# Kernel optimization log

Measured on AMD Instinct MI355X. Metric: run time of the kernel, lower is better.

The kernel has to match this reference:

```python
import jax, jax.numpy as jnp
import numpy as np
from jax import lax

NPOINT = 1024
RADIUS = 0.2
NSAMPLE = 32
BN_EPS = 1e-5


def _gather(points, idx):
    # points [B,N,C], idx [B,S] or [B,S,K] -> [B,S,C] / [B,S,K,C]
    return jax.vmap(lambda p, i: p[i])(points, idx)


def farthest_point_sample(xyz, npoint):
    # xyz [B,N,3] -> idx [B,npoint]; deterministic start at index 0
    B, N, _ = xyz.shape

    def step(carry, _):
        distance, farthest = carry
        centroid = jnp.take_along_axis(xyz, farthest[:, None, None], axis=1)  # [B,1,3]
        dist = jnp.sum((xyz - centroid) ** 2, axis=-1)  # [B,N]
        distance = jnp.minimum(distance, dist)
        nxt = jnp.argmax(distance, axis=1).astype(jnp.int32)
        return (distance, nxt), farthest

    init = (jnp.full((B, N), 1e10, xyz.dtype), jnp.zeros((B,), jnp.int32))
    _, cents = lax.scan(step, init, None, length=npoint)  # [npoint,B]
    return cents.T  # [B,npoint]


def query_ball_point(radius, nsample, xyz, new_xyz):
    # xyz [B,N,3], new_xyz [B,S,3] -> idx [B,S,nsample]
    B, N, _ = xyz.shape
    sqrdists = (jnp.sum(new_xyz ** 2, -1, keepdims=True)
                - 2.0 * jnp.einsum('bsc,bnc->bsn', new_xyz, xyz)
                + jnp.sum(xyz ** 2, -1)[:, None, :])  # [B,S,N]
    idx = jnp.where(sqrdists > radius * radius, N, jnp.arange(N, dtype=jnp.int32)[None, None, :])
    idx = jnp.sort(idx, axis=-1)[:, :, :nsample]
    first = idx[:, :, :1]
    idx = jnp.where(idx == N, first, idx)
    return jnp.minimum(idx, N - 1)


def _mlp_bn_relu_stack(x, params):
    # x [B,S,K,C]; 1x1 conv == per-point linear; BN in training mode (batch stats)
    for (w, b, g, bt) in params:
        x = jnp.einsum('bskc,oc->bsko', x, w) + b
        mean = jnp.mean(x, axis=(0, 1, 2))
        var = jnp.var(x, axis=(0, 1, 2))
        x = g * (x - mean) * lax.rsqrt(var + BN_EPS) + bt
        x = jax.nn.relu(x)
    return x


def setup_inputs() -> dict:
    key = jax.random.key(0)
    ks = jax.random.split(key, 8)
    B, N, D = 16, 4096, 64
    xyz = jax.random.uniform(ks[0], (B, N, 3), dtype=jnp.float32)
    points = jax.random.normal(ks[1], (B, N, D), dtype=jnp.float32)
    chans = [67, 64, 64, 128]
    inp = {"xyz": xyz, "points": points}
    for i in range(3):
        cin, cout = chans[i], chans[i + 1]
        inp[f"w{i+1}"] = jax.random.normal(ks[2 + i], (cout, cin), dtype=jnp.float32) * 0.05
        inp[f"b{i+1}"] = jnp.zeros((cout,), jnp.float32)
        inp[f"g{i+1}"] = jnp.ones((cout,), jnp.float32)
        inp[f"bt{i+1}"] = jnp.zeros((cout,), jnp.float32)
    return inp


def reference(xyz, points, w1, b1, g1, bt1, w2, b2, g2, bt2, w3, b3, g3, bt3):
    B, N, _ = xyz.shape
    fps_idx = farthest_point_sample(xyz, NPOINT)  # [B,S]
    new_xyz = _gather(xyz, fps_idx)  # [B,S,3]
    gidx = query_ball_point(RADIUS, NSAMPLE, xyz, new_xyz)  # [B,S,K]
    grouped_xyz = _gather(xyz, gidx) - new_xyz[:, :, None, :]  # [B,S,K,3]
    feat = jnp.concatenate([grouped_xyz, _gather(points, gidx)], axis=-1)  # [B,S,K,67]
    params = [(w1, b1, g1, bt1), (w2, b2, g2, bt2), (w3, b3, g3, bt3)]
    feat = _mlp_bn_relu_stack(feat, params)  # [B,S,K,128]
    new_points = jnp.max(feat, axis=2)  # [B,S,128]
    return (new_xyz, new_points)
```

## Files before the change

kernel.cpp:

```cpp
#include <hip/hip_runtime.h>
#include <cstdint>

#define NB 16
#define NN 4096
#define ND 64
#define NPOINT 1024
#define NSAMPLE 32
#define NROWS (NB * NPOINT * NSAMPLE)
#define BN_EPS 1e-5f
#define NSLOT 32
#define LD 68

#define OFF_GIDX   0
#define OFF_STATS  (2 * 1024 * 1024)
#define OFF_MAX    (OFF_STATS + 131072)
#define OFF_MIN    (OFF_MAX + 8388608)
#define MED_TOTAL  ((size_t)OFF_MIN + 8388608)
#define SMALL_TOTAL ((size_t)OFF_MAX)
#define OFF_Y2BF   MED_TOTAL
#define BIG_TOTAL  (OFF_Y2BF + (size_t)NROWS * 64 * 2)
#define OFF_Y1BF   BIG_TOTAL
#define BIG2_TOTAL (OFF_Y1BF + (size_t)NROWS * 64 * 2)

#define S1SUM 0
#define S1SQ  2048
#define S2SUM 4096
#define S2SQ  6144
#define S3SUM 8192
#define S3SQ  12288
#define A3OFF 16384
#define C3OFF 16512

__device__ __forceinline__ unsigned short f2bf(float f) {
    const unsigned u = __float_as_uint(f);
    return (unsigned short)((u + 0x7FFFu + ((u >> 16) & 1u)) >> 16);
}
__device__ __forceinline__ float bf2f(unsigned short s) {
    return __uint_as_float(((unsigned)s) << 16);
}

__global__ __launch_bounds__(256) void fps_kernel(const float* __restrict__ xyz,
                                                  float* __restrict__ out_newxyz) {
    __shared__ float pxyz[NN * 3];
    __shared__ unsigned long long skey[2][4];
    __shared__ float sxyz[2][4][3];
    const int b = blockIdx.x, tid = threadIdx.x;
    const int wave = tid >> 6, lane = tid & 63;
    const float* base = xyz + (size_t)b * NN * 3;

    for (int i = tid; i < NN * 3 / 4; i += 256)
        reinterpret_cast<float4*>(pxyz)[i] = reinterpret_cast<const float4*>(base)[i];
    __syncthreads();

    float X[16], Y[16], Z[16], D[16];
#pragma unroll
    for (int k = 0; k < 16; ++k) {
        const int p = k * 256 + tid;
        X[k] = pxyz[3 * p + 0];
        Y[k] = pxyz[3 * p + 1];
        Z[k] = pxyz[3 * p + 2];
        D[k] = 1e10f;
    }

    float cx = pxyz[0], cy = pxyz[1], cz = pxyz[2];
    float* outb = out_newxyz + (size_t)b * NPOINT * 3;

    for (int it = 0; it < NPOINT; ++it) {
        if (tid == 0) {
            outb[it * 3 + 0] = cx;
            outb[it * 3 + 1] = cy;
            outb[it * 3 + 2] = cz;
        }
        float bv = -1.0f;
        int   bi = 0;
#pragma unroll
        for (int k = 0; k < 16; ++k) {
            const float dx = __fsub_rn(X[k], cx);
            const float dy = __fsub_rn(Y[k], cy);
            const float dz = __fsub_rn(Z[k], cz);
            const float d  = __fadd_rn(__fadd_rn(__fmul_rn(dx, dx), __fmul_rn(dy, dy)),
                                       __fmul_rn(dz, dz));
            const float nd = fminf(D[k], d);
            D[k] = nd;
            if (nd > bv) { bv = nd; bi = k * 256 + tid; }
        }
        unsigned long long key =
            ((unsigned long long)__float_as_uint(bv) << 32) | (unsigned)(~bi);
#pragma unroll
        for (int off = 32; off >= 1; off >>= 1) {
            const unsigned long long ok = __shfl_xor(key, off);
            key = (ok > key) ? ok : key;
        }
        const int par = it & 1;
        if (lane == 0) {
            const int widx = (int)(~(unsigned)key);
            skey[par][wave] = key;
            sxyz[par][wave][0] = pxyz[3 * widx + 0];
            sxyz[par][wave][1] = pxyz[3 * widx + 1];
            sxyz[par][wave][2] = pxyz[3 * widx + 2];
        }
        __syncthreads();
        unsigned long long k0 = skey[par][0], k1 = skey[par][1];
        unsigned long long k2 = skey[par][2], k3 = skey[par][3];
        float ax = sxyz[par][0][0], ay = sxyz[par][0][1], az = sxyz[par][0][2];
        const float bx = sxyz[par][1][0], by = sxyz[par][1][1], bz = sxyz[par][1][2];
        float ex = sxyz[par][2][0], ey = sxyz[par][2][1], ez = sxyz[par][2][2];
        const float fx = sxyz[par][3][0], fy = sxyz[par][3][1], fz = sxyz[par][3][2];
        if (k1 > k0) { k0 = k1; ax = bx; ay = by; az = bz; }
        if (k3 > k2) { k2 = k3; ex = fx; ey = fy; ez = fz; }
        if (k2 > k0) { ax = ex; ay = ey; az = ez; }
        cx = ax; cy = ay; cz = az;
    }
}

__global__ __launch_bounds__(256) void query_kernel(const float* __restrict__ xyz,
                                                    const float* __restrict__ newxyz,
                                                    int* __restrict__ gidx) {
    const int gtid = blockIdx.x * 256 + threadIdx.x;
    const int q    = gtid >> 6;
    const int lane = threadIdx.x & 63;
    if (q >= NB * NPOINT) return;
    const int b = q >> 10;
    const float* xb = xyz + (size_t)b * NN * 3;
    const float cx = newxyz[q * 3 + 0];
    const float cy = newxyz[q * 3 + 1];
    const float cz = newxyz[q * 3 + 2];
    const float snew = __fadd_rn(__fadd_rn(__fmul_rn(cx, cx), __fmul_rn(cy, cy)),
                                 __fmul_rn(cz, cz));
    const float rsq = (float)(0.2 * 0.2);
    int* outq = gidx + (size_t)q * NSAMPLE;

    int count = 0, first = 0;
    for (int base = 0; base < NN; base += 128) {
        const int pA = base + lane, pB = base + 64 + lane;
        const float xA = xb[pA * 3 + 0], yA = xb[pA * 3 + 1], zA = xb[pA * 3 + 2];
        const float xB = xb[pB * 3 + 0], yB = xb[pB * 3 + 1], zB = xb[pB * 3 + 2];
        const float sxA = __fadd_rn(__fadd_rn(__fmul_rn(xA, xA), __fmul_rn(yA, yA)),
                                    __fmul_rn(zA, zA));
        const float sxB = __fadd_rn(__fadd_rn(__fmul_rn(xB, xB), __fmul_rn(yB, yB)),
                                    __fmul_rn(zB, zB));
        float dotA = __fmul_rn(cx, xA);
        dotA = fmaf(cy, yA, dotA);
        dotA = fmaf(cz, zA, dotA);
        float dotB = __fmul_rn(cx, xB);
        dotB = fmaf(cy, yB, dotB);
        dotB = fmaf(cz, zB, dotB);
        const float sqA = __fadd_rn(__fsub_rn(snew, __fadd_rn(dotA, dotA)), sxA);
        const float sqB = __fadd_rn(__fsub_rn(snew, __fadd_rn(dotB, dotB)), sxB);
        const bool qualA = !(sqA > rsq);
        const bool qualB = !(sqB > rsq);
        const unsigned long long maskA = __ballot(qualA);
        const unsigned long long maskB = __ballot(qualB);
        if (count == 0) {
            if (maskA)      first = base + (int)__builtin_ctzll(maskA);
            else if (maskB) first = base + 64 + (int)__builtin_ctzll(maskB);
        }
        const unsigned long long below = (1ull << lane) - 1ull;
        const int cA = __popcll(maskA);
        if (qualA) {
            const int pos = count + __popcll(maskA & below);
            if (pos < NSAMPLE) outq[pos] = pA;
        }
        if (qualB) {
            const int pos = count + cA + __popcll(maskB & below);
            if (pos < NSAMPLE) outq[pos] = pB;
        }
        count += cA + __popcll(maskB);
        if (count >= NSAMPLE) break;
    }
    if (count < NSAMPLE) {
        for (int pos = count + lane; pos < NSAMPLE; pos += 64) outq[pos] = first;
    }
}

__device__ __forceinline__ void stage64(const float* __restrict__ xyz,
                                        const float* __restrict__ points,
                                        const float* __restrict__ newxyz,
                                        const int* __restrict__ gidx,
                                        int row0, int tid, float* featT) {
    const int rl = tid >> 2, qd = tid & 3;
    const int R   = row0 + rl;
    const int grp = R >> 5;
    const int idx = gidx[R];
    const int b   = grp >> 10;
    const float* prow = points + ((size_t)b * NN + idx) * ND + qd * 16;
#pragma unroll
    for (int j = 0; j < 4; ++j) {
        const float4 v = *reinterpret_cast<const float4*>(prow + j * 4);
        const int k = 3 + qd * 16 + j * 4;
        featT[(k + 0) * LD + rl] = v.x;
        featT[(k + 1) * LD + rl] = v.y;
        featT[(k + 2) * LD + rl] = v.z;
        featT[(k + 3) * LD + rl] = v.w;
    }
    if (qd == 0) {
        const float* xr = xyz + ((size_t)b * NN + idx) * 3;
        const float* cr = newxyz + (size_t)grp * 3;
        featT[0 * LD + rl] = xr[0] - cr[0];
        featT[1 * LD + rl] = xr[1] - cr[1];
        featT[2 * LD + rl] = xr[2] - cr[2];
    }
}

__device__ __forceinline__ void fold64(const float* __restrict__ ssum,
                                       const float* __restrict__ ssq,
                                       const float* __restrict__ g,
                                       const float* __restrict__ bt,
                                       int tid, float* a_s, float* c_s) {
    if (tid < 64) {
        float s = 0.f, q = 0.f;
#pragma unroll
        for (int sl = 0; sl < NSLOT; ++sl) { s += ssum[sl * 64 + tid]; q += ssq[sl * 64 + tid]; }
        const float Ninv = 1.0f / (float)NROWS;
        const float mean = s * Ninv;
        const float var  = fmaf(-mean, mean, q * Ninv);
        const float a    = g[tid] * rsqrtf(var + BN_EPS);
        a_s[tid] = a;
        c_s[tid] = bt[tid] - mean * a;
    }
}

template<int CIN>
__device__ __forceinline__ void mm_bnrelu(const float* __restrict__ w,
                                          const float* __restrict__ bias,
                                          const float* inT, float* outT,
                                          const float* a_s, const float* c_s, int tid) {
    const int c = tid & 63, rg = tid >> 6;
    float wr[CIN];
#pragma unroll
    for (int k = 0; k < CIN; ++k) wr[k] = w[c * CIN + k];
    const float bv = bias[c];
    const float av = a_s[c], cv = c_s[c];
#pragma unroll
    for (int bat = 0; bat < 2; ++bat) {
        const int rb = rg * 16 + bat * 8;
        float acc[8];
#pragma unroll
        for (int j = 0; j < 8; ++j) acc[j] = bv;
#pragma unroll
        for (int k = 0; k < CIN; ++k) {
            float f[8];
            *reinterpret_cast<float4*>(&f[0]) = *reinterpret_cast<const float4*>(&inT[k * LD + rb]);
            *reinterpret_cast<float4*>(&f[4]) = *reinterpret_cast<const float4*>(&inT[k * LD + rb + 4]);
            const float wv = wr[k];
#pragma unroll
            for (int j = 0; j < 8; ++j) acc[j] = fmaf(f[j], wv, acc[j]);
        }
        float o[8];
#pragma unroll
        for (int j = 0; j < 8; ++j) o[j] = fmaxf(0.f, fmaf(av, acc[j], cv));
        *reinterpret_cast<float4*>(&outT[c * LD + rb])     = *reinterpret_cast<float4*>(&o[0]);
        *reinterpret_cast<float4*>(&outT[c * LD + rb + 4]) = *reinterpret_cast<float4*>(&o[4]);
    }
}

template<bool ST>
__global__ __launch_bounds__(256) void pass1_kernel(
    const float* __restrict__ xyz, const float* __restrict__ points,
    const float* __restrict__ newxyz, const int* __restrict__ gidx,
    const float* __restrict__ w1, const float* __restrict__ b1,
    float* __restrict__ stats, unsigned short* __restrict__ y1bf) {
    __shared__ float featT[67 * LD];
    __shared__ float red[4][64], redq[4][64];
    const int tid = threadIdx.x, blk = blockIdx.x;
    stage64(xyz, points, newxyz, gidx, blk * 64, tid, featT);
    __syncthreads();
    const int c = tid & 63, rg = tid >> 6;
    float wr[67];
#pragma unroll
    for (int k = 0; k < 67; ++k) wr[k] = w1[c * 67 + k];
    const float bv = b1[c];
    float ssum = 0.f, ssq = 0.f;
#pragma unroll
    for (int bat = 0; bat < 2; ++bat) {
        const int rb = rg * 16 + bat * 8;
        float acc[8];
#pragma unroll
        for (int j = 0; j < 8; ++j) acc[j] = bv;
#pragma unroll
        for (int k = 0; k < 67; ++k) {
            float f[8];
            *reinterpret_cast<float4*>(&f[0]) = *reinterpret_cast<const float4*>(&featT[k * LD + rb]);
            *reinterpret_cast<float4*>(&f[4]) = *reinterpret_cast<const float4*>(&featT[k * LD + rb + 4]);
            const float wv = wr[k];
#pragma unroll
            for (int j = 0; j < 8; ++j) acc[j] = fmaf(f[j], wv, acc[j]);
        }
        if (ST) {
            unsigned short o[8];
#pragma unroll
            for (int j = 0; j < 8; ++j) o[j] = f2bf(acc[j]);
            *reinterpret_cast<uint4*>(&y1bf[(size_t)blk * 4096 + c * 64 + rb]) =
                *reinterpret_cast<uint4*>(o);
        }
#pragma unroll
        for (int j = 0; j < 8; ++j) { ssum += acc[j]; ssq = fmaf(acc[j], acc[j], ssq); }
    }
    red[rg][c] = ssum;
    redq[rg][c] = ssq;
    __syncthreads();
    if (tid < 64) {
        const float s = red[0][tid] + red[1][tid] + red[2][tid] + red[3][tid];
        const float q = redq[0][tid] + redq[1][tid] + redq[2][tid] + redq[3][tid];
        const int slot = blk & (NSLOT - 1);
        atomicAdd(&stats[S1SUM + slot * 64 + tid], s);
        atomicAdd(&stats[S1SQ + slot * 64 + tid], q);
    }
}

__global__ __launch_bounds__(256) void pass2big_kernel(
    const unsigned short* __restrict__ y1bf,
    const float* __restrict__ g1, const float* __restrict__ bt1,
    const float* __restrict__ w2, const float* __restrict__ b2,
    float* __restrict__ stats, unsigned short* __restrict__ y2bf) {
    __shared__ float t1T[64 * LD];
    __shared__ float a1s[64], c1s[64];
    __shared__ float red[4][64], redq[4][64];
    const int tid = threadIdx.x, blk = blockIdx.x;
    fold64(stats + S1SUM, stats + S1SQ, g1, bt1, tid, a1s, c1s);
    __syncthreads();
    {
        const int cch = tid >> 2, r0 = (tid & 3) * 16;
        const float a1 = a1s[cch], c1 = c1s[cch];
        const uint4 u0 = *reinterpret_cast<const uint4*>(&y1bf[(size_t)blk * 4096 + cch * 64 + r0]);
        const uint4 u1 = *reinterpret_cast<const uint4*>(&y1bf[(size_t)blk * 4096 + cch * 64 + r0 + 8]);
        const unsigned short* us0 = reinterpret_cast<const unsigned short*>(&u0);
        const unsigned short* us1 = reinterpret_cast<const unsigned short*>(&u1);
#pragma unroll
        for (int j = 0; j < 8; ++j) {
            t1T[cch * LD + r0 + j]     = fmaxf(0.f, fmaf(a1, bf2f(us0[j]), c1));
            t1T[cch * LD + r0 + 8 + j] = fmaxf(0.f, fmaf(a1, bf2f(us1[j]), c1));
        }
    }
    __syncthreads();
    const int c = tid & 63, rg = tid >> 6;
    float wr[64];
#pragma unroll
    for (int k = 0; k < 64; ++k) wr[k] = w2[c * 64 + k];
    const float bv = b2[c];
    float ssum = 0.f, ssq = 0.f;
#pragma unroll
    for (int bat = 0; bat < 2; ++bat) {
        const int rb = rg * 16 + bat * 8;
        float acc[8];
#pragma unroll
        for (int j = 0; j < 8; ++j) acc[j] = bv;
#pragma unroll
        for (int k = 0; k < 64; ++k) {
            float f[8];
            *reinterpret_cast<float4*>(&f[0]) = *reinterpret_cast<const float4*>(&t1T[k * LD + rb]);
            *reinterpret_cast<float4*>(&f[4]) = *reinterpret_cast<const float4*>(&t1T[k * LD + rb + 4]);
            const float wv = wr[k];
#pragma unroll
            for (int j = 0; j < 8; ++j) acc[j] = fmaf(f[j], wv, acc[j]);
        }
        {
            unsigned short o[8];
#pragma unroll
            for (int j = 0; j < 8; ++j) o[j] = f2bf(acc[j]);
            *reinterpret_cast<uint4*>(&y2bf[(size_t)blk * 4096 + c * 64 + rb]) =
                *reinterpret_cast<uint4*>(o);
        }
#pragma unroll
        for (int j = 0; j < 8; ++j) { ssum += acc[j]; ssq = fmaf(acc[j], acc[j], ssq); }
    }
    red[rg][c] = ssum;
    redq[rg][c] = ssq;
    __syncthreads();
    if (tid < 64) {
        const float s = red[0][tid] + red[1][tid] + red[2][tid] + red[3][tid];
        const float q = redq[0][tid] + redq[1][tid] + redq[2][tid] + redq[3][tid];
        const int slot = blk & (NSLOT - 1);
        atomicAdd(&stats[S2SUM + slot * 64 + tid], s);
        atomicAdd(&stats[S2SQ + slot * 64 + tid], q);
    }
}

template<bool ST>
__global__ __launch_bounds__(256) void pass2_kernel(
    const float* __restrict__ xyz, const float* __restrict__ points,
    const float* __restrict__ newxyz, const int* __restrict__ gidx,
    const float* __restrict__ w1, const float* __restrict__ b1,
    const float* __restrict__ g1, const float* __restrict__ bt1,
    const float* __restrict__ w2, const float* __restrict__ b2,
    float* __restrict__ stats, unsigned short* __restrict__ y2bf) {
    __shared__ float featT[67 * LD];
    __shared__ float t1T[64 * LD];
    __shared__ float a1s[64], c1s[64];
    __shared__ float red[4][64], redq[4][64];
    const int tid = threadIdx.x, blk = blockIdx.x;
    fold64(stats + S1SUM, stats + S1SQ, g1, bt1, tid, a1s, c1s);
    stage64(xyz, points, newxyz, gidx, blk * 64, tid, featT);
    __syncthreads();
    mm_bnrelu<67>(w1, b1, featT, t1T, a1s, c1s, tid);
    __syncthreads();
    const int c = tid & 63, rg = tid >> 6;
    float wr[64];
#pragma unroll
    for (int k = 0; k < 64; ++k) wr[k] = w2[c * 64 + k];
    const float bv = b2[c];
    float ssum = 0.f, ssq = 0.f;
#pragma unroll
    for (int bat = 0; bat < 2; ++bat) {
        const int rb = rg * 16 + bat * 8;
        float acc[8];
#pragma unroll
        for (int j = 0; j < 8; ++j) acc[j] = bv;
#pragma unroll
        for (int k = 0; k < 64; ++k) {
            float f[8];
            *reinterpret_cast<float4*>(&f[0]) = *reinterpret_cast<const float4*>(&t1T[k * LD + rb]);
            *reinterpret_cast<float4*>(&f[4]) = *reinterpret_cast<const float4*>(&t1T[k * LD + rb + 4]);
            const float wv = wr[k];
#pragma unroll
            for (int j = 0; j < 8; ++j) acc[j] = fmaf(f[j], wv, acc[j]);
        }
        if (ST) {
            unsigned short o[8];
#pragma unroll
            for (int j = 0; j < 8; ++j) o[j] = f2bf(acc[j]);
            *reinterpret_cast<uint4*>(&y2bf[(size_t)blk * 4096 + c * 64 + rb]) =
                *reinterpret_cast<uint4*>(o);
        }
#pragma unroll
        for (int j = 0; j < 8; ++j) { ssum += acc[j]; ssq = fmaf(acc[j], acc[j], ssq); }
    }
    red[rg][c] = ssum;
    redq[rg][c] = ssq;
    __syncthreads();
    if (tid < 64) {
        const float s = red[0][tid] + red[1][tid] + red[2][tid] + red[3][tid];
        const float q = redq[0][tid] + redq[1][tid] + redq[2][tid] + redq[3][tid];
        const int slot = blk & (NSLOT - 1);
        atomicAdd(&stats[S2SUM + slot * 64 + tid], s);
        atomicAdd(&stats[S2SQ + slot * 64 + tid], q);
    }
}

__global__ __launch_bounds__(256) void pass3big_kernel(
    const unsigned short* __restrict__ y2bf,
    const float* __restrict__ g2, const float* __restrict__ bt2,
    const float* __restrict__ w3, const float* __restrict__ b3,
    float* __restrict__ stats, float* __restrict__ maxbuf, float* __restrict__ minbuf) {
    __shared__ float t2T[64 * LD];
    __shared__ float a2s[64], c2s[64];
    __shared__ float redM[4][128], redm[4][128], redS[4][128], redQ[4][128];
    const int tid = threadIdx.x, blk = blockIdx.x;
    fold64(stats + S2SUM, stats + S2SQ, g2, bt2, tid, a2s, c2s);
    __syncthreads();
    {
        const int cch = tid >> 2, r0 = (tid & 3) * 16;
        const float a2 = a2s[cch], c2 = c2s[cch];
        const uint4 u0 = *reinterpret_cast<const uint4*>(&y2bf[(size_t)blk * 4096 + cch * 64 + r0]);
        const uint4 u1 = *reinterpret_cast<const uint4*>(&y2bf[(size_t)blk * 4096 + cch * 64 + r0 + 8]);
        const unsigned short* us0 = reinterpret_cast<const unsigned short*>(&u0);
        const unsigned short* us1 = reinterpret_cast<const unsigned short*>(&u1);
#pragma unroll
        for (int j = 0; j < 8; ++j) {
            t2T[cch * LD + r0 + j]     = fmaxf(0.f, fmaf(a2, bf2f(us0[j]), c2));
            t2T[cch * LD + r0 + 8 + j] = fmaxf(0.f, fmaf(a2, bf2f(us1[j]), c2));
        }
    }
    __syncthreads();

    const int c0 = tid & 63, rg2 = tid >> 6;
    const int rb = rg2 * 16;
    float acc0[16], acc1[16];
    const float bv0 = b3[c0], bv1 = b3[c0 + 64];
#pragma unroll
    for (int j = 0; j < 16; ++j) { acc0[j] = bv0; acc1[j] = bv1; }
    for (int half = 0; half < 2; ++half) {
        float wr0[32], wr1[32];
#pragma unroll
        for (int k = 0; k < 32; ++k) {
            wr0[k] = w3[c0 * 64 + half * 32 + k];
            wr1[k] = w3[(c0 + 64) * 64 + half * 32 + k];
        }
#pragma unroll
        for (int k = 0; k < 32; ++k) {
            const int kk = half * 32 + k;
            float f[16];
            *reinterpret_cast<float4*>(&f[0])  = *reinterpret_cast<const float4*>(&t2T[kk * LD + rb]);
            *reinterpret_cast<float4*>(&f[4])  = *reinterpret_cast<const float4*>(&t2T[kk * LD + rb + 4]);
            *reinterpret_cast<float4*>(&f[8])  = *reinterpret_cast<const float4*>(&t2T[kk * LD + rb + 8]);
            *reinterpret_cast<float4*>(&f[12]) = *reinterpret_cast<const float4*>(&t2T[kk * LD + rb + 12]);
            const float w0 = wr0[k], w1v = wr1[k];
#pragma unroll
            for (int j = 0; j < 16; ++j) {
                acc0[j] = fmaf(f[j], w0, acc0[j]);
                acc1[j] = fmaf(f[j], w1v, acc1[j]);
            }
        }
    }
    float maxv0 = -3.4e38f, minv0 = 3.4e38f, ssum0 = 0.f, ssq0 = 0.f;
    float maxv1 = -3.4e38f, minv1 = 3.4e38f, ssum1 = 0.f, ssq1 = 0.f;
#pragma unroll
    for (int j = 0; j < 16; ++j) {
        maxv0 = fmaxf(maxv0, acc0[j]); minv0 = fminf(minv0, acc0[j]);
        ssum0 += acc0[j]; ssq0 = fmaf(acc0[j], acc0[j], ssq0);
        maxv1 = fmaxf(maxv1, acc1[j]); minv1 = fminf(minv1, acc1[j]);
        ssum1 += acc1[j]; ssq1 = fmaf(acc1[j], acc1[j], ssq1);
    }
    redM[rg2][c0] = maxv0; redM[rg2][c0 + 64] = maxv1;
    redm[rg2][c0] = minv0; redm[rg2][c0 + 64] = minv1;
    redS[rg2][c0] = ssum0; redS[rg2][c0 + 64] = ssum1;
    redQ[rg2][c0] = ssq0;  redQ[rg2][c0 + 64] = ssq1;
    __syncthreads();
    {
        const int g2i = tid >> 7, cc = tid & 127;
        const int g = blk * 2 + g2i;
        maxbuf[(size_t)g * 128 + cc] = fmaxf(redM[2 * g2i][cc], redM[2 * g2i + 1][cc]);
        minbuf[(size_t)g * 128 + cc] = fminf(redm[2 * g2i][cc], redm[2 * g2i + 1][cc]);
    }
    if (tid < 128) {
        const float s = (redS[0][tid] + redS[1][tid]) + (redS[2][tid] + redS[3][tid]);
        const float q = (redQ[0][tid] + redQ[1][tid]) + (redQ[2][tid] + redQ[3][tid]);
        const int slot = blk & (NSLOT - 1);
        atomicAdd(&stats[S3SUM + slot * 128 + tid], s);
        atomicAdd(&stats[S3SQ + slot * 128 + tid], q);
    }
}

template<bool MM>
__global__ __launch_bounds__(256) void pass3_kernel(
    const float* __restrict__ xyz, const float* __restrict__ points,
    const float* __restrict__ newxyz, const int* __restrict__ gidx,
    const float* __restrict__ w1, const float* __restrict__ b1,
    const float* __restrict__ g1, const float* __restrict__ bt1,
    const float* __restrict__ w2, const float* __restrict__ b2,
    const float* __restrict__ g2, const float* __restrict__ bt2,
    const float* __restrict__ w3, const float* __restrict__ b3,
    float* __restrict__ stats, float* __restrict__ maxbuf, float* __restrict__ minbuf) {
    __shared__ float bufA[67 * LD];
    __shared__ float t1T[64 * LD];
    __shared__ float a1s[64], c1s[64], a2s[64], c2s[64];
    __shared__ float redM[4][128], redm[4][128], redS[4][128], redQ[4][128];
    const int tid = threadIdx.x, blk = blockIdx.x;
    fold64(stats + S1SUM, stats + S1SQ, g1, bt1, tid, a1s, c1s);
    fold64(stats + S2SUM, stats + S2SQ, g2, bt2, tid, a2s, c2s);
    stage64(xyz, points, newxyz, gidx, blk * 64, tid, bufA);
    __syncthreads();
    mm_bnrelu<67>(w1, b1, bufA, t1T, a1s, c1s, tid);
    __syncthreads();
    mm_bnrelu<64>(w2, b2, t1T, bufA, a2s, c2s, tid);
    __syncthreads();

    const int c0 = tid & 63, rg2 = tid >> 6;
    const int rb = rg2 * 16;
    float acc0[16], acc1[16];
    const float bv0 = b3[c0], bv1 = b3[c0 + 64];
#pragma unroll
    for (int j = 0; j < 16; ++j) { acc0[j] = bv0; acc1[j] = bv1; }
    for (int half = 0; half < 2; ++half) {
        float wr0[32], wr1[32];
#pragma unroll
        for (int k = 0; k < 32; ++k) {
            wr0[k] = w3[c0 * 64 + half * 32 + k];
            wr1[k] = w3[(c0 + 64) * 64 + half * 32 + k];
        }
#pragma unroll
        for (int k = 0; k < 32; ++k) {
            const int kk = half * 32 + k;
            float f[16];
            *reinterpret_cast<float4*>(&f[0])  = *reinterpret_cast<const float4*>(&bufA[kk * LD + rb]);
            *reinterpret_cast<float4*>(&f[4])  = *reinterpret_cast<const float4*>(&bufA[kk * LD + rb + 4]);
            *reinterpret_cast<float4*>(&f[8])  = *reinterpret_cast<const float4*>(&bufA[kk * LD + rb + 8]);
            *reinterpret_cast<float4*>(&f[12]) = *reinterpret_cast<const float4*>(&bufA[kk * LD + rb + 12]);
            const float w0 = wr0[k], w1v = wr1[k];
#pragma unroll
            for (int j = 0; j < 16; ++j) {
                acc0[j] = fmaf(f[j], w0, acc0[j]);
                acc1[j] = fmaf(f[j], w1v, acc1[j]);
            }
        }
    }
    float maxv0 = -3.4e38f, minv0 = 3.4e38f, ssum0 = 0.f, ssq0 = 0.f;
    float maxv1 = -3.4e38f, minv1 = 3.4e38f, ssum1 = 0.f, ssq1 = 0.f;
#pragma unroll
    for (int j = 0; j < 16; ++j) {
        maxv0 = fmaxf(maxv0, acc0[j]); minv0 = fminf(minv0, acc0[j]);
        ssum0 += acc0[j]; ssq0 = fmaf(acc0[j], acc0[j], ssq0);
        maxv1 = fmaxf(maxv1, acc1[j]); minv1 = fminf(minv1, acc1[j]);
        ssum1 += acc1[j]; ssq1 = fmaf(acc1[j], acc1[j], ssq1);
    }
    redM[rg2][c0] = maxv0; redM[rg2][c0 + 64] = maxv1;
    redm[rg2][c0] = minv0; redm[rg2][c0 + 64] = minv1;
    redS[rg2][c0] = ssum0; redS[rg2][c0 + 64] = ssum1;
    redQ[rg2][c0] = ssq0;  redQ[rg2][c0 + 64] = ssq1;
    __syncthreads();
    if (MM) {
        const int g2i = tid >> 7, cc = tid & 127;
        const int g = blk * 2 + g2i;
        maxbuf[(size_t)g * 128 + cc] = fmaxf(redM[2 * g2i][cc], redM[2 * g2i + 1][cc]);
        minbuf[(size_t)g * 128 + cc] = fminf(redm[2 * g2i][cc], redm[2 * g2i + 1][cc]);
    }
    if (tid < 128) {
        const float s = (redS[0][tid] + redS[1][tid]) + (redS[2][tid] + redS[3][tid]);
        const float q = (redQ[0][tid] + redQ[1][tid]) + (redQ[2][tid] + redQ[3][tid]);
        const int slot = blk & (NSLOT - 1);
        atomicAdd(&stats[S3SUM + slot * 128 + tid], s);
        atomicAdd(&stats[S3SQ + slot * 128 + tid], q);
    }
}

__global__ __launch_bounds__(256) void pass4_kernel(
    const float* __restrict__ xyz, const float* __restrict__ points,
    const float* __restrict__ newxyz, const int* __restrict__ gidx,
    const float* __restrict__ w1, const float* __restrict__ b1,
    const float* __restrict__ g1, const float* __restrict__ bt1,
    const float* __restrict__ w2, const float* __restrict__ b2,
    const float* __restrict__ g2, const float* __restrict__ bt2,
    const float* __restrict__ w3, const float* __restrict__ b3,
    const float* __restrict__ g3, const float* __restrict__ bt3,
    const float* __restrict__ stats, float* __restrict__ outp) {
    __shared__ float bufA[67 * LD];
    __shared__ float t1T[64 * LD];
    __shared__ float a1s[64], c1s[64], a2s[64], c2s[64];
    __shared__ float a3s[128], c3s[128];
    const int tid = threadIdx.x, blk = blockIdx.x;
    fold64(stats + S1SUM, stats + S1SQ, g1, bt1, tid, a1s, c1s);
    fold64(stats + S2SUM, stats + S2SQ, g2, bt2, tid, a2s, c2s);
    if (tid < 128) {
        float s = 0.f, q = 0.f;
#pragma unroll
        for (int sl = 0; sl < NSLOT; ++sl) { s += stats[S3SUM + sl * 128 + tid]; q += stats[S3SQ + sl * 128 + tid]; }
        const float Ninv = 1.0f / (float)NROWS;
        const float mean = s * Ninv;
        const float var  = fmaf(-mean, mean, q * Ninv);
        const float a    = g3[tid] * rsqrtf(var + BN_EPS);
        a3s[tid] = a;
        c3s[tid] = bt3[tid] - mean * a;
    }
    stage64(xyz, points, newxyz, gidx, blk * 64, tid, bufA);
    __syncthreads();
    mm_bnrelu<67>(w1, b1, bufA, t1T, a1s, c1s, tid);
    __syncthreads();
    mm_bnrelu<64>(w2, b2, t1T, bufA, a2s, c2s, tid);
    __syncthreads();

    const int c2 = tid & 127, rg2 = tid >> 7;
    float wr[64];
#pragma unroll
    for (int k = 0; k < 64; ++k) wr[k] = w3[c2 * 64 + k];
    const float bv = b3[c2];
    const float av = a3s[c2], cv = c3s[c2];
    float maxv = -3.4e38f;
#pragma unroll
    for (int bat = 0; bat < 4; ++bat) {
        const int rb = rg2 * 32 + bat * 8;
        float acc[8];
#pragma unroll
        for (int j = 0; j < 8; ++j) acc[j] = bv;
#pragma unroll
        for (int k = 0; k < 64; ++k) {
            float f[8];
            *reinterpret_cast<float4*>(&f[0]) = *reinterpret_cast<const float4*>(&bufA[k * LD + rb]);
            *reinterpret_cast<float4*>(&f[4]) = *reinterpret_cast<const float4*>(&bufA[k * LD + rb + 4]);
            const float wv = wr[k];
#pragma unroll
            for (int j = 0; j < 8; ++j) acc[j] = fmaf(f[j], wv, acc[j]);
        }
#pragma unroll
        for (int j = 0; j < 8; ++j) maxv = fmaxf(maxv, fmaxf(0.f, fmaf(av, acc[j], cv)));
    }
    const int g = blk * 2 + rg2;
    outp[(size_t)g * 128 + c2] = maxv;
}

__global__ void derive3_kernel(const float* __restrict__ g3, const float* __restrict__ bt3,
                               float* __restrict__ stats) {
    const int c = threadIdx.x;
    float s = 0.f, q = 0.f;
#pragma unroll
    for (int sl = 0; sl < NSLOT; ++sl) { s += stats[S3SUM + sl * 128 + c]; q += stats[S3SQ + sl * 128 + c]; }
    const float Ninv = 1.0f / (float)NROWS;
    const float mean = s * Ninv;
    const float var  = fmaf(-mean, mean, q * Ninv);
    const float a    = g3[c] * rsqrtf(var + BN_EPS);
    stats[A3OFF + c] = a;
    stats[C3OFF + c] = bt3[c] - mean * a;
}

__global__ __launch_bounds__(256) void final_kernel(
    const float* __restrict__ maxbuf, const float* __restrict__ minbuf,
    const float* __restrict__ stats, float* __restrict__ outp) {
    const int gid = blockIdx.x * 256 + threadIdx.x;
    if (gid >= NB * NPOINT * 128) return;
    const int c = gid & 127;
    const float a  = stats[A3OFF + c];
    const float cc = stats[C3OFF + c];
    const float v  = (a >= 0.f) ? maxbuf[gid] : minbuf[gid];
    outp[gid] = fmaxf(0.f, fmaf(a, v, cc));
}

extern "C" void kernel_launch(void* const* d_in, const int* in_sizes, int n_in,
                              void* d_out, int out_size, void* d_ws, size_t ws_size,
                              hipStream_t stream) {
    const float* xyz    = (const float*)d_in[0];
    const float* points = (const float*)d_in[1];
    const float* w1 = (const float*)d_in[2];
    const float* b1 = (const float*)d_in[3];
    const float* g1 = (const float*)d_in[4];
    const float* bt1 = (const float*)d_in[5];
    const float* w2 = (const float*)d_in[6];
    const float* b2 = (const float*)d_in[7];
    const float* g2 = (const float*)d_in[8];
    const float* bt2 = (const float*)d_in[9];
    const float* w3 = (const float*)d_in[10];
    const float* b3 = (const float*)d_in[11];
    const float* g3 = (const float*)d_in[12];
    const float* bt3 = (const float*)d_in[13];

    float* out_newxyz = (float*)d_out;
    float* out_newpts = (float*)d_out + NB * NPOINT * 3;

    char* ws = (char*)d_ws;
    if (ws_size < SMALL_TOTAL) return;

    int*   gidx   = (int*)(ws + OFF_GIDX);
    float* stats  = (float*)(ws + OFF_STATS);
    float* maxbuf = (float*)(ws + OFF_MAX);
    float* minbuf = (float*)(ws + OFF_MIN);
    unsigned short* y2bf = (unsigned short*)(ws + OFF_Y2BF);
    unsigned short* y1bf = (unsigned short*)(ws + OFF_Y1BF);
    const bool med  = (ws_size >= MED_TOTAL);
    const bool big  = (ws_size >= BIG_TOTAL);
    const bool big2 = (ws_size >= BIG2_TOTAL);

    hipMemsetAsync(stats, 0, 65536, stream);

    fps_kernel<<<NB, 256, 0, stream>>>(xyz, out_newxyz);
    query_kernel<<<(NB * NPOINT * 64) / 256, 256, 0, stream>>>(xyz, out_newxyz, gidx);
    if (big2) {
        pass1_kernel<true><<<NROWS / 64, 256, 0, stream>>>(xyz, points, out_newxyz, gidx,
                                                           w1, b1, stats, y1bf);
        pass2big_kernel<<<NROWS / 64, 256, 0, stream>>>(y1bf, g1, bt1, w2, b2, stats, y2bf);
        pass3big_kernel<<<NROWS / 64, 256, 0, stream>>>(y2bf, g2, bt2, w3, b3,
                                                        stats, maxbuf, minbuf);
        derive3_kernel<<<1, 128, 0, stream>>>(g3, bt3, stats);
        final_kernel<<<(NB * NPOINT * 128) / 256, 256, 0, stream>>>(maxbuf, minbuf, stats, out_newpts);
    } else if (big) {
        pass1_kernel<false><<<NROWS / 64, 256, 0, stream>>>(xyz, points, out_newxyz, gidx,
                                                            w1, b1, stats, y1bf);
        pass2_kernel<true><<<NROWS / 64, 256, 0, stream>>>(xyz, points, out_newxyz, gidx,
                                                           w1, b1, g1, bt1, w2, b2, stats, y2bf);
        pass3big_kernel<<<NROWS / 64, 256, 0, stream>>>(y2bf, g2, bt2, w3, b3,
                                                        stats, maxbuf, minbuf);
        derive3_kernel<<<1, 128, 0, stream>>>(g3, bt3, stats);
        final_kernel<<<(NB * NPOINT * 128) / 256, 256, 0, stream>>>(maxbuf, minbuf, stats, out_newpts);
    } else if (med) {
        pass1_kernel<false><<<NROWS / 64, 256, 0, stream>>>(xyz, points, out_newxyz, gidx,
                                                            w1, b1, stats, y1bf);
        pass2_kernel<false><<<NROWS / 64, 256, 0, stream>>>(xyz, points, out_newxyz, gidx,
                                                            w1, b1, g1, bt1, w2, b2, stats, y2bf);
        pass3_kernel<true><<<NROWS / 64, 256, 0, stream>>>(xyz, points, out_newxyz, gidx,
                                                           w1, b1, g1, bt1, w2, b2, g2, bt2,
                                                           w3, b3, stats, maxbuf, minbuf);
        derive3_kernel<<<1, 128, 0, stream>>>(g3, bt3, stats);
        final_kernel<<<(NB * NPOINT * 128) / 256, 256, 0, stream>>>(maxbuf, minbuf, stats, out_newpts);
    } else {
        pass1_kernel<false><<<NROWS / 64, 256, 0, stream>>>(xyz, points, out_newxyz, gidx,
                                                            w1, b1, stats, y1bf);
        pass2_kernel<false><<<NROWS / 64, 256, 0, stream>>>(xyz, points, out_newxyz, gidx,
                                                            w1, b1, g1, bt1, w2, b2, stats, y2bf);
        pass3_kernel<false><<<NROWS / 64, 256, 0, stream>>>(xyz, points, out_newxyz, gidx,
                                                            w1, b1, g1, bt1, w2, b2, g2, bt2,
                                                            w3, b3, stats, maxbuf, minbuf);
        pass4_kernel<<<NROWS / 64, 256, 0, stream>>>(xyz, points, out_newxyz, gidx,
                                                     w1, b1, g1, bt1, w2, b2, g2, bt2,
                                                     w3, b3, g3, bt3, stats, out_newpts);
    }
}
```

Baseline: 1.193 ms.

## Widen FPS block to 512 threads and simplify per-iteration argmax reduction

The farthest-point-sampling kernel now runs 512 threads per batch, so each thread holds 8 points, assigned contiguously, instead of 16 strided ones. The 64-bit key shuffle reduction becomes a float max shuffle followed by a ballot and lane lookup. Each wave publishes one float4 slot, and every thread scans 8 slots to pick the winner. This shortens the serial per-iteration chain in the 1024-step loop. It may change tie-breaking: lowest lane first, and a strict greater-than across waves favours lower waves. Contiguous indexing keeps lowest-index ties in order.

```diff
diff --git a/kernel.cpp b/kernel.cpp
--- a/kernel.cpp
+++ b/kernel.cpp
@@ -39,23 +39,22 @@
     return __uint_as_float(((unsigned)s) << 16);
 }
 
-__global__ __launch_bounds__(256) void fps_kernel(const float* __restrict__ xyz,
+__global__ __launch_bounds__(512) void fps_kernel(const float* __restrict__ xyz,
                                                   float* __restrict__ out_newxyz) {
     __shared__ float pxyz[NN * 3];
-    __shared__ unsigned long long skey[2][4];
-    __shared__ float sxyz[2][4][3];
+    __shared__ float4 slot[2][8];
     const int b = blockIdx.x, tid = threadIdx.x;
     const int wave = tid >> 6, lane = tid & 63;
     const float* base = xyz + (size_t)b * NN * 3;
 
-    for (int i = tid; i < NN * 3 / 4; i += 256)
+    for (int i = tid; i < NN * 3 / 4; i += 512)
         reinterpret_cast<float4*>(pxyz)[i] = reinterpret_cast<const float4*>(base)[i];
     __syncthreads();
 
-    float X[16], Y[16], Z[16], D[16];
-#pragma unroll
-    for (int k = 0; k < 16; ++k) {
-        const int p = k * 256 + tid;
+    float X[8], Y[8], Z[8], D[8];
+#pragma unroll
+    for (int k = 0; k < 8; ++k) {
+        const int p = tid * 8 + k;
         X[k] = pxyz[3 * p + 0];
         Y[k] = pxyz[3 * p + 1];
         Z[k] = pxyz[3 * p + 2];
@@ -74,7 +73,7 @@
         float bv = -1.0f;
         int   bi = 0;
 #pragma unroll
-        for (int k = 0; k < 16; ++k) {
+        for (int k = 0; k < 8; ++k) {
             const float dx = __fsub_rn(X[k], cx);
             const float dy = __fsub_rn(Y[k], cy);
             const float dz = __fsub_rn(Z[k], cz);
@@ -82,34 +81,29 @@
                                        __fmul_rn(dz, dz));
             const float nd = fminf(D[k], d);
             D[k] = nd;
-            if (nd > bv) { bv = nd; bi = k * 256 + tid; }
-        }
-        unsigned long long key =
-            ((unsigned long long)__float_as_uint(bv) << 32) | (unsigned)(~bi);
-#pragma unroll
-        for (int off = 32; off >= 1; off >>= 1) {
-            const unsigned long long ok = __shfl_xor(key, off);
-            key = (ok > key) ? ok : key;
-        }
+            if (nd > bv) { bv = nd; bi = tid * 8 + k; }
+        }
+        const float lv = bv;
+#pragma unroll
+        for (int off = 32; off >= 1; off >>= 1)
+            bv = fmaxf(bv, __shfl_xor(bv, off));
+        const unsigned long long mask = __ballot(lv == bv);
+        const int src  = (int)__builtin_ctzll(mask);
+        const int widx = __shfl(bi, src);
         const int par = it & 1;
         if (lane == 0) {
-            const int widx = (int)(~(unsigned)key);
-            skey[par][wave] = key;
-            sxyz[par][wave][0] = pxyz[3 * widx + 0];
-            sxyz[par][wave][1] = pxyz[3 * widx + 1];
-            sxyz[par][wave][2] = pxyz[3 * widx + 2];
+            slot[par][wave] = make_float4(bv, pxyz[3 * widx + 0],
+                                              pxyz[3 * widx + 1],
+                                              pxyz[3 * widx + 2]);
         }
         __syncthreads();
-        unsigned long long k0 = skey[par][0], k1 = skey[par][1];
-        unsigned long long k2 = skey[par][2], k3 = skey[par][3];
-        float ax = sxyz[par][0][0], ay = sxyz[par][0][1], az = sxyz[par][0][2];
-        const float bx = sxyz[par][1][0], by = sxyz[par][1][1], bz = sxyz[par][1][2];
-        float ex = sxyz[par][2][0], ey = sxyz[par][2][1], ez = sxyz[par][2][2];
-        const float fx = sxyz[par][3][0], fy = sxyz[par][3][1], fz = sxyz[par][3][2];
-        if (k1 > k0) { k0 = k1; ax = bx; ay = by; az = bz; }
-        if (k3 > k2) { k2 = k3; ex = fx; ey = fy; ez = fz; }
-        if (k2 > k0) { ax = ex; ay = ey; az = ez; }
-        cx = ax; cy = ay; cz = az;
+        float4 best = slot[par][0];
+#pragma unroll
+        for (int w = 1; w < 8; ++w) {
+            const float4 s = slot[par][w];
+            if (s.x > best.x) best = s;
+        }
+        cx = best.y; cy = best.z; cz = best.w;
     }
 }
 
@@ -729,7 +723,7 @@
 
     hipMemsetAsync(stats, 0, 65536, stream);
 
-    fps_kernel<<<NB, 256, 0, stream>>>(xyz, out_newxyz);
+    fps_kernel<<<NB, 512, 0, stream>>>(xyz, out_newxyz);
     query_kernel<<<(NB * NPOINT * 64) / 256, 256, 0, stream>>>(xyz, out_newxyz, gidx);
     if (big2) {
         pass1_kernel<true><<<NROWS / 64, 256, 0, stream>>>(xyz, points, out_newxyz, gidx,
```

Result: slower. 1.398 ms (+17.3%).
